# Performance work log

Measured on AMD Instinct MI355X. Metric: run time of the kernel, lower is better.

Reference implementation:

```python
import jax, jax.numpy as jnp
import numpy as np

B, N, E = 1024, 40, 64
P = N * (N - 1) // 2  # 780 field pairs


def _pair_indices(n):
    row, col = [], []
    for i in range(n - 1):
        for j in range(i + 1, n):
            row.append(i)
            col.append(j)
    return np.asarray(row), np.asarray(col)


def setup_inputs() -> dict:
    key = jax.random.key(0)
    k1, k2 = jax.random.split(key)
    inputs = jax.random.normal(k1, (B, N, E), dtype=jnp.float32)
    # xavier-normal-ish init for the 'mat' kernel (E, P, E)
    std = float(np.sqrt(2.0 / (E + E)))
    param = jax.random.normal(k2, (E, P, E), dtype=jnp.float32) * std
    return {"inputs": inputs, "param": param}


def reference(inputs, param):
    n = inputs.shape[1]
    rowidx, colidx = _pair_indices(n)
    p = inputs[:, rowidx]  # (B, P, E)
    q = inputs[:, colidx]  # (B, P, E)
    # torch: kp = (p[:,None] * param).sum(-1).transpose(1,2); out = (kp*q).sum(-1)
    # == out[b,i] = sum_{e,f} p[b,i,e] * param[f,i,e] * q[b,i,f]
    out = jnp.einsum('bie,fie,bif->bi', p, param, q)
    return out[:, None, :]  # (B, 1, P)
```

## Files before the change

### kernel.cpp

```cpp
#include <hip/hip_runtime.h>

namespace {
constexpr int kB = 1024;
constexpr int kN = 40;
constexpr int kE = 64;
constexpr int kP = kN * (kN - 1) / 2;

using bf16x8 = __attribute__((ext_vector_type(8))) short;
using f32x4  = __attribute__((ext_vector_type(4))) float;

__device__ inline unsigned short f2bf(float x) {
  union { float f; unsigned u; } v; v.f = x;
  return (unsigned short)((v.u + 0x7FFFu + ((v.u >> 16) & 1u)) >> 16);
}
__device__ inline float bf2f(unsigned short u) {
  union { unsigned u; float f; } v; v.u = (unsigned)u << 16;
  return v.f;
}

__global__ __launch_bounds__(256) void cvt_frag(const float* __restrict__ in,
                                                unsigned short* __restrict__ xf) {
  const int n    = blockIdx.x;
  const int bgc  = blockIdx.y;
  const int t    = threadIdx.x;
  const int bgl  = t >> 6;
  const int L    = t & 63;
  const int col  = L & 15;
  const int quad = L >> 4;
  const int b    = (bgc * 4 + bgl) * 16 + col;
  const float* src    = in + ((size_t)b * kN + n) * kE + quad * 8;
  unsigned short* dst = xf + (((size_t)n * 64 + bgc * 4 + bgl) << 10) + L * 8;
  const float4 v0 = ((const float4*)src)[0];
  const float4 v1 = ((const float4*)src)[1];
  const float4 v2 = ((const float4*)(src + 32))[0];
  const float4 v3 = ((const float4*)(src + 32))[1];
  bf16x8 o0, o1;
  o0[0] = (short)f2bf(v0.x); o0[1] = (short)f2bf(v0.y);
  o0[2] = (short)f2bf(v0.z); o0[3] = (short)f2bf(v0.w);
  o0[4] = (short)f2bf(v1.x); o0[5] = (short)f2bf(v1.y);
  o0[6] = (short)f2bf(v1.z); o0[7] = (short)f2bf(v1.w);
  o1[0] = (short)f2bf(v2.x); o1[1] = (short)f2bf(v2.y);
  o1[2] = (short)f2bf(v2.z); o1[3] = (short)f2bf(v2.w);
  o1[4] = (short)f2bf(v3.x); o1[5] = (short)f2bf(v3.y);
  o1[6] = (short)f2bf(v3.z); o1[7] = (short)f2bf(v3.w);
  *(bf16x8*)dst         = o0;
  *(bf16x8*)(dst + 512) = o1;
}

__global__ __launch_bounds__(256, 4)
void opn_pair(const unsigned short* __restrict__ xf,
              const float* __restrict__ param,
              float* __restrict__ out) {
  __shared__ short Ms[2 * 64 * 72];
  __shared__ float dots[256 * 2];

  const int t    = threadIdx.x;
  const int w    = t >> 6;
  const int L    = t & 63;
  const int col  = L & 15;
  const int quad = L >> 4;

  int tx = blockIdx.x, r = 0;
  for (;;) { const int nq = (40 - r) >> 1; if (tx < nq) break; tx -= nq; ++r; }
  const int c0  = r + 1 + tx * 2;
  const int ib  = r * (79 - r) / 2 + c0 - r - 1;
  const int gb0 = blockIdx.y * 256;

  {
    const int pp  = t >> 7;
    const int sub = t & 127;
    const int f   = sub >> 1;
    const int eh  = sub & 1;
    if (c0 + pp <= kN - 1) {
      const float* src = param + ((size_t)f * kP + (ib + pp)) * kE + eh * 32;
      short* d = &Ms[pp * 4608 + f * 72 + eh * 32];
#pragma unroll
      for (int c8 = 0; c8 < 4; ++c8) {
        const float4 a0 = ((const float4*)src)[c8 * 2];
        const float4 a1 = ((const float4*)src)[c8 * 2 + 1];
        bf16x8 o;
        o[0] = (short)f2bf(a0.x); o[1] = (short)f2bf(a0.y);
        o[2] = (short)f2bf(a0.z); o[3] = (short)f2bf(a0.w);
        o[4] = (short)f2bf(a1.x); o[5] = (short)f2bf(a1.y);
        o[6] = (short)f2bf(a1.z); o[7] = (short)f2bf(a1.w);
        *(bf16x8*)(d + c8 * 8) = o;
      }
    }
  }
  __syncthreads();

  const int cc = w & 1;
  const int h  = w >> 1;
  const int c  = c0 + cc;

  if (c <= kN - 1) {
    bf16x8 A[4][2];
#pragma unroll
    for (int mt = 0; mt < 4; ++mt)
#pragma unroll
      for (int ks = 0; ks < 2; ++ks)
        A[mt][ks] = *(const bf16x8*)&Ms[cc * 4608 + (16 * mt + col) * 72 + ks * 32 + quad * 8];

    const int bgg0 = blockIdx.y * 16 + h * 8;
    const unsigned short* pb = xf + (((size_t)r * 64 + bgg0) << 10);
    const unsigned short* qb = xf + (((size_t)c * 64 + bgg0) << 10);
    const int qoff = (quad >> 1) * 128 + col * 8 + (quad & 1) * 4;

    bf16x8 B0[2], B1[2];
    ushort4 Q[2][4];
    B0[0]   = *(const bf16x8*)(pb + L * 8);
    B1[0]   = *(const bf16x8*)(pb + 512 + L * 8);
    Q[0][0] = *(const ushort4*)(qb + qoff);
    Q[0][1] = *(const ushort4*)(qb + 256 + qoff);
    Q[0][2] = *(const ushort4*)(qb + 512 + qoff);
    Q[0][3] = *(const ushort4*)(qb + 768 + qoff);

#pragma unroll
    for (int bg = 0; bg < 8; ++bg) {
      const int cb = bg & 1, nb = cb ^ 1;
      if (bg < 7) {
        const unsigned short* pn = pb + ((size_t)(bg + 1) << 10);
        const unsigned short* qn = qb + ((size_t)(bg + 1) << 10);
        B0[nb]   = *(const bf16x8*)(pn + L * 8);
        B1[nb]   = *(const bf16x8*)(pn + 512 + L * 8);
        Q[nb][0] = *(const ushort4*)(qn + qoff);
        Q[nb][1] = *(const ushort4*)(qn + 256 + qoff);
        Q[nb][2] = *(const ushort4*)(qn + 512 + qoff);
        Q[nb][3] = *(const ushort4*)(qn + 768 + qoff);
      }
      f32x4 acc[4];
#pragma unroll
      for (int mt = 0; mt < 4; ++mt) acc[mt] = (f32x4){0.f, 0.f, 0.f, 0.f};
#pragma unroll
      for (int mt = 0; mt < 4; ++mt) {
        acc[mt] = __builtin_amdgcn_mfma_f32_16x16x32_bf16(A[mt][0], B0[cb], acc[mt], 0, 0, 0);
        acc[mt] = __builtin_amdgcn_mfma_f32_16x16x32_bf16(A[mt][1], B1[cb], acc[mt], 0, 0, 0);
      }
      float s[4];
#pragma unroll
      for (int mt = 0; mt < 4; ++mt) {
        const ushort4 qu = Q[cb][mt];
        float sm;
        sm = acc[mt][0] * bf2f(qu.x);
        sm = fmaf(acc[mt][1], bf2f(qu.y), sm);
        sm = fmaf(acc[mt][2], bf2f(qu.z), sm);
        sm = fmaf(acc[mt][3], bf2f(qu.w), sm);
        s[mt] = sm;
      }
      float dot = (s[0] + s[1]) + (s[2] + s[3]);
      dot += __shfl_xor(dot, 16, 64);
      dot += __shfl_xor(dot, 32, 64);
      if (quad == 0) dots[(h * 128 + bg * 16 + col) * 2 + cc] = dot;
    }
  }
  __syncthreads();

  const float2 dv = *(const float2*)&dots[t * 2];
  float* ob = out + (size_t)(gb0 + t) * kP + ib;
  ob[0] = dv.x;
  if (c0 + 1 <= kN - 1) ob[1] = dv.y;
}

__global__ __launch_bounds__(256, 2)
void opn_fp32(const float* __restrict__ inp, const float* __restrict__ param,
              float* __restrict__ out) {
  const int i    = blockIdx.x;
  const int wave = threadIdx.x >> 6;
  const int lane = threadIdx.x & 63;
  const int b    = (blockIdx.y * 4 + wave) * 64 + lane;
  int rem = i, r = 0;
  while (rem >= kN - 1 - r) { rem -= kN - 1 - r; ++r; }
  const int c = r + 1 + rem;
  const float* pb = inp + (size_t)b * (kN * kE) + r * kE;
  const float* qb = inp + (size_t)b * (kN * kE) + c * kE;
  float p[kE];
#pragma unroll
  for (int e = 0; e < kE; ++e) p[e] = pb[e];
  float acc = 0.f;
  for (int f = 0; f < kE; ++f) {
    const float* Mrow = param + ((size_t)f * kP + i) * kE;
    float t0 = 0.f, t1 = 0.f, t2 = 0.f, t3 = 0.f;
#pragma unroll
    for (int e = 0; e < kE; e += 4) {
      t0 = fmaf(Mrow[e + 0], p[e + 0], t0);
      t1 = fmaf(Mrow[e + 1], p[e + 1], t1);
      t2 = fmaf(Mrow[e + 2], p[e + 2], t2);
      t3 = fmaf(Mrow[e + 3], p[e + 3], t3);
    }
    acc = fmaf((t0 + t1) + (t2 + t3), qb[f], acc);
  }
  out[(size_t)b * kP + i] = acc;
}
}

extern "C" void kernel_launch(void* const* d_in, const int* in_sizes, int n_in,
                              void* d_out, int out_size, void* d_ws, size_t ws_size,
                              hipStream_t stream) {
  const float* inputs = (const float*)d_in[0];
  const float* param  = (const float*)d_in[1];
  float* out          = (float*)d_out;

  const size_t xf_bytes = (size_t)kN * kB * kE * sizeof(unsigned short);

  if (ws_size >= xf_bytes) {
    unsigned short* xf = (unsigned short*)d_ws;
    cvt_frag<<<dim3(kN, 16), 256, 0, stream>>>(inputs, xf);
    opn_pair<<<dim3(400, 4), 256, 0, stream>>>(xf, param, out);
  } else {
    opn_fp32<<<dim3(kP, 4), 256, 0, stream>>>(inputs, param, out);
  }
}
```

Before: 90.01 us.

## Pre-convert param to bf16 MFMA fragments once in a merged prep kernel

Before this change, each opn_pair block converted its param slices from fp32 to bf16 through shared memory, and each param slice was re-read and re-converted by all 4 blockIdx.y blocks. A merged prep kernel now converts the inputs and also writes param into a workspace, already packed into MFMA A-fragment layout. The main kernel then loads A fragments directly from global memory, with no shared staging and no barrier. This adds a workspace write and read-back of about 6 MB, but cuts the fp32 param reads by a factor of four and merges the two prep launches into one.

```diff
diff --git a/kernel.cpp b/kernel.cpp
--- a/kernel.cpp
+++ b/kernel.cpp
@@ -18,40 +18,67 @@
   return v.f;
 }
 
-__global__ __launch_bounds__(256) void cvt_frag(const float* __restrict__ in,
-                                                unsigned short* __restrict__ xf) {
-  const int n    = blockIdx.x;
-  const int bgc  = blockIdx.y;
-  const int t    = threadIdx.x;
-  const int bgl  = t >> 6;
-  const int L    = t & 63;
-  const int col  = L & 15;
-  const int quad = L >> 4;
-  const int b    = (bgc * 4 + bgl) * 16 + col;
-  const float* src    = in + ((size_t)b * kN + n) * kE + quad * 8;
-  unsigned short* dst = xf + (((size_t)n * 64 + bgc * 4 + bgl) << 10) + L * 8;
-  const float4 v0 = ((const float4*)src)[0];
-  const float4 v1 = ((const float4*)src)[1];
-  const float4 v2 = ((const float4*)(src + 32))[0];
-  const float4 v3 = ((const float4*)(src + 32))[1];
-  bf16x8 o0, o1;
-  o0[0] = (short)f2bf(v0.x); o0[1] = (short)f2bf(v0.y);
-  o0[2] = (short)f2bf(v0.z); o0[3] = (short)f2bf(v0.w);
-  o0[4] = (short)f2bf(v1.x); o0[5] = (short)f2bf(v1.y);
-  o0[6] = (short)f2bf(v1.z); o0[7] = (short)f2bf(v1.w);
-  o1[0] = (short)f2bf(v2.x); o1[1] = (short)f2bf(v2.y);
-  o1[2] = (short)f2bf(v2.z); o1[3] = (short)f2bf(v2.w);
-  o1[4] = (short)f2bf(v3.x); o1[5] = (short)f2bf(v3.y);
-  o1[6] = (short)f2bf(v3.z); o1[7] = (short)f2bf(v3.w);
-  *(bf16x8*)dst         = o0;
-  *(bf16x8*)(dst + 512) = o1;
+__global__ __launch_bounds__(256) void prep(const float* __restrict__ in,
+                                            const float* __restrict__ param,
+                                            unsigned short* __restrict__ xf,
+                                            unsigned short* __restrict__ Af) {
+  __shared__ short Ms[64 * 72];
+  const int t = threadIdx.x;
+  if (blockIdx.x < 640) {
+    const int n    = blockIdx.x >> 4;
+    const int bgc  = blockIdx.x & 15;
+    const int bgl  = t >> 6;
+    const int L    = t & 63;
+    const int col  = L & 15;
+    const int quad = L >> 4;
+    const int b    = (bgc * 4 + bgl) * 16 + col;
+    const float* src    = in + ((size_t)b * kN + n) * kE + quad * 8;
+    unsigned short* dst = xf + (((size_t)n * 64 + bgc * 4 + bgl) << 10) + L * 8;
+    const float4 v0 = ((const float4*)src)[0];
+    const float4 v1 = ((const float4*)src)[1];
+    const float4 v2 = ((const float4*)(src + 32))[0];
+    const float4 v3 = ((const float4*)(src + 32))[1];
+    bf16x8 o0, o1;
+    o0[0] = (short)f2bf(v0.x); o0[1] = (short)f2bf(v0.y);
+    o0[2] = (short)f2bf(v0.z); o0[3] = (short)f2bf(v0.w);
+    o0[4] = (short)f2bf(v1.x); o0[5] = (short)f2bf(v1.y);
+    o0[6] = (short)f2bf(v1.z); o0[7] = (short)f2bf(v1.w);
+    o1[0] = (short)f2bf(v2.x); o1[1] = (short)f2bf(v2.y);
+    o1[2] = (short)f2bf(v2.z); o1[3] = (short)f2bf(v2.w);
+    o1[4] = (short)f2bf(v3.x); o1[5] = (short)f2bf(v3.y);
+    o1[6] = (short)f2bf(v3.z); o1[7] = (short)f2bf(v3.w);
+    *(bf16x8*)dst         = o0;
+    *(bf16x8*)(dst + 512) = o1;
+  } else {
+    const int i = blockIdx.x - 640;
+#pragma unroll
+    for (int ph = 0; ph < 4; ++ph) {
+      const int f  = ph * 16 + (t >> 4);
+      const int e0 = (t & 15) * 4;
+      const float4 v = *(const float4*)(param + ((size_t)f * kP + i) * kE + e0);
+      short* d = &Ms[f * 72 + e0];
+      d[0] = (short)f2bf(v.x); d[1] = (short)f2bf(v.y);
+      d[2] = (short)f2bf(v.z); d[3] = (short)f2bf(v.w);
+    }
+    __syncthreads();
+    unsigned short* base = Af + (size_t)i * 4096;
+#pragma unroll
+    for (int u = 0; u < 2; ++u) {
+      const int chunk = t * 2 + u;
+      const int L    = chunk & 63;
+      const int mtks = chunk >> 6;
+      const int mt   = mtks >> 1, ks = mtks & 1;
+      const int col  = L & 15, quad = L >> 4;
+      const bf16x8 a = *(const bf16x8*)&Ms[(16 * mt + col) * 72 + ks * 32 + quad * 8];
+      *(bf16x8*)(base + chunk * 8) = a;
+    }
+  }
 }
 
 __global__ __launch_bounds__(256, 4)
-void opn_pair(const unsigned short* __restrict__ xf,
-              const float* __restrict__ param,
-              float* __restrict__ out) {
-  __shared__ short Ms[2 * 64 * 72];
+void opn_pair2(const unsigned short* __restrict__ xf,
+               const unsigned short* __restrict__ Af,
+               float* __restrict__ out) {
   __shared__ float dots[256 * 2];
 
   const int t    = threadIdx.x;
@@ -66,40 +93,18 @@
   const int ib  = r * (79 - r) / 2 + c0 - r - 1;
   const int gb0 = blockIdx.y * 256;
 
-  {
-    const int pp  = t >> 7;
-    const int sub = t & 127;
-    const int f   = sub >> 1;
-    const int eh  = sub & 1;
-    if (c0 + pp <= kN - 1) {
-      const float* src = param + ((size_t)f * kP + (ib + pp)) * kE + eh * 32;
-      short* d = &Ms[pp * 4608 + f * 72 + eh * 32];
-#pragma unroll
-      for (int c8 = 0; c8 < 4; ++c8) {
-        const float4 a0 = ((const float4*)src)[c8 * 2];
-        const float4 a1 = ((const float4*)src)[c8 * 2 + 1];
-        bf16x8 o;
-        o[0] = (short)f2bf(a0.x); o[1] = (short)f2bf(a0.y);
-        o[2] = (short)f2bf(a0.z); o[3] = (short)f2bf(a0.w);
-        o[4] = (short)f2bf(a1.x); o[5] = (short)f2bf(a1.y);
-        o[6] = (short)f2bf(a1.z); o[7] = (short)f2bf(a1.w);
-        *(bf16x8*)(d + c8 * 8) = o;
-      }
-    }
-  }
-  __syncthreads();
-
   const int cc = w & 1;
   const int h  = w >> 1;
   const int c  = c0 + cc;
 
   if (c <= kN - 1) {
+    const unsigned short* ab = Af + (size_t)(ib + cc) * 4096 + L * 8;
     bf16x8 A[4][2];
 #pragma unroll
     for (int mt = 0; mt < 4; ++mt)
 #pragma unroll
       for (int ks = 0; ks < 2; ++ks)
-        A[mt][ks] = *(const bf16x8*)&Ms[cc * 4608 + (16 * mt + col) * 72 + ks * 32 + quad * 8];
+        A[mt][ks] = *(const bf16x8*)(ab + (mt * 2 + ks) * 512);
 
     const int bgg0 = blockIdx.y * 16 + h * 8;
     const unsigned short* pb = xf + (((size_t)r * 64 + bgg0) << 10);
@@ -201,11 +206,13 @@
   float* out          = (float*)d_out;
 
   const size_t xf_bytes = (size_t)kN * kB * kE * sizeof(unsigned short);
-
-  if (ws_size >= xf_bytes) {
+  const size_t af_bytes = (size_t)kP * 4096 * sizeof(unsigned short);
+
+  if (ws_size >= xf_bytes + af_bytes) {
     unsigned short* xf = (unsigned short*)d_ws;
-    cvt_frag<<<dim3(kN, 16), 256, 0, stream>>>(inputs, xf);
-    opn_pair<<<dim3(400, 4), 256, 0, stream>>>(xf, param, out);
+    unsigned short* Af = (unsigned short*)((char*)d_ws + xf_bytes);
+    prep<<<640 + kP, 256, 0, stream>>>(inputs, param, xf, Af);
+    opn_pair2<<<dim3(400, 4), 256, 0, stream>>>(xf, Af, out);
   } else {
     opn_fp32<<<dim3(kP, 4), 256, 0, stream>>>(inputs, param, out);
   }
```

Result: no change. 89.38 us (-0.7%).
